# Kernel tuning notes

Hardware: AMD Instinct MI355X
Metric: run time of the kernel (lower is better)

Reference implementation:

```python
import jax, jax.numpy as jnp
import numpy as np

N, F, D = 32, 1024, 512
H = 2 * D  # dim * ratio
EPS = 1e-5


def batchnorm1d(x, gamma, beta):
    # x: (N, F, L); BatchNorm1d over channel dim F, stats over (N, L) (training mode, biased var)
    mean = jnp.mean(x, axis=(0, 2), keepdims=True)
    var = jnp.var(x, axis=(0, 2), keepdims=True)
    xn = (x - mean) * jax.lax.rsqrt(var + EPS)
    return xn * gamma[None, :, None] + beta[None, :, None]


def setup_inputs() -> dict:
    key = jax.random.key(0)
    ks = jax.random.split(key, 5)
    x = jax.random.normal(ks[0], (N, F, D), dtype=jnp.float32)
    W0 = jax.random.normal(ks[1], (H, D), dtype=jnp.float32) * 0.02  # Linear(D->H) weight (out,in)
    b0 = jnp.zeros((H,), jnp.float32)
    W1 = jax.random.normal(ks[2], (D, H), dtype=jnp.float32) * 0.02  # Linear(H->D)
    b1 = jnp.zeros((D,), jnp.float32)
    Wc = jax.random.normal(ks[3], (F, F), dtype=jnp.float32) * 0.02  # Conv1d k=1 weight (out_ch,in_ch)
    bc = jnp.zeros((F,), jnp.float32)
    ones = jnp.ones((F,), jnp.float32)
    zeros = jnp.zeros((F,), jnp.float32)
    return {
        "x": x,
        "W0": W0, "b0": b0, "g0": ones, "be0": zeros,
        "W1": W1, "b1": b1, "g1": ones, "be1": zeros,
        "gf": ones, "bf": zeros,
        "Wc": Wc, "bc": bc,
        "go": ones, "bo": zeros,
    }


def reference(x, W0, b0, g0, be0, W1, b1, g1, be1, gf, bf, Wc, bc, go, bo):
    # proj_mlp0: Linear(D->H) + BN1d(F)
    v = jnp.einsum('nfd,hd->nfh', x, W0) + b0  # (N, F, H)
    v = batchnorm1d(v, g0, be0)
    # correlation: bmm(v, v^T) -> softsign -> bmm(w, v)
    w = jnp.einsum('nfh,ngh->nfg', v, v)  # (N, F, F)
    w = w / (1.0 + jnp.abs(w))  # softsign
    v = jnp.einsum('nfg,ngh->nfh', w, v)  # (N, F, H)
    # proj_mlp1: Linear(H->D) + BN1d(F)
    v = jnp.einsum('nfh,dh->nfd', v, W1) + b1  # (N, F, D)
    v = batchnorm1d(v, g1, be1)
    # feed_norm(v + x)
    xr = batchnorm1d(v + x, gf, bf)
    # proj_conv: Conv1d(F->F, kernel=1) over channel dim
    v = jnp.einsum('oi,nid->nod', Wc, xr) + bc[None, :, None]
    return batchnorm1d(v + xr, go, bo)
```

## Files before the change

kernel.cpp:

```cpp
#include <hip/hip_runtime.h>
#include <stdint.h>

#define NB 32
#define FC 1024
#define DD 512
#define HH 1024
#define BN_EPS 1e-5f

typedef unsigned short u16;
typedef unsigned int u32;
typedef __attribute__((ext_vector_type(8))) short bf16x8;
typedef __attribute__((ext_vector_type(4))) float f32x4;
typedef __attribute__((ext_vector_type(8))) unsigned short ushort8v;

#define AS1 __attribute__((address_space(1)))
#define AS3 __attribute__((address_space(3)))

__device__ __forceinline__ float b2f(u16 u) {
    union { u32 i; float f; } v;
    v.i = ((u32)u) << 16;
    return v.f;
}
__device__ __forceinline__ u16 f2b(float f) {
    union { float f; u32 i; } v;
    v.f = f;
    const u32 b = v.i;
    return (u16)((b + 0x7FFFu + ((b >> 16) & 1u)) >> 16);
}

__device__ __forceinline__ void gld16(const u16* g, u16* l) {
    __builtin_amdgcn_global_load_lds((const AS1 u32*)g, (AS3 u32*)l, 16, 0, 0);
}

__device__ __forceinline__ void swizzle_tiles(int& mt, int& nt, int& zt) {
    const int gx = gridDim.x, gy = gridDim.y, gz = gridDim.z;
    const int mzTot = gy * gz;
    if ((mzTot & 7) != 0) { nt = blockIdx.x; mt = blockIdx.y; zt = blockIdx.z; return; }
    long lin = ((long)blockIdx.z * gy + blockIdx.y) * gx + blockIdx.x;
    const int slab = mzTot >> 3;
    const int xcd = (int)(lin & 7);
    const long idx = lin >> 3;
    nt = (int)(idx % gx);
    const int mz = (int)(idx / gx) + xcd * slab;
    mt = mz % gy;
    zt = mz / gy;
}

__global__ __launch_bounds__(256) void detect_dtype(
    const u32* __restrict__ x, int* __restrict__ flag)
{
    __shared__ int cnt[256];
    int c = 0;
    for (int i = threadIdx.x; i < 4096; i += 256) {
        const u32 lo = x[i] & 0xFFFFu;
        const u32 e = (lo >> 7) & 0xFFu;
        if (e >= 0x68u && e <= 0x85u) c++;
    }
    cnt[threadIdx.x] = c;
    __syncthreads();
    for (int s = 128; s > 0; s >>= 1) {
        if (threadIdx.x < (unsigned)s) cnt[threadIdx.x] += cnt[threadIdx.x + s];
        __syncthreads();
    }
    if (threadIdx.x == 0) flag[0] = (cnt[0] > 2048) ? 1 : 0;
}

__global__ __launch_bounds__(256) void zero_partials(float* __restrict__ sp) {
    sp[blockIdx.x * 256 + threadIdx.x] = 0.0f;
}

__global__ __launch_bounds__(256) void fold_bn(
    const float* __restrict__ sp, const u16* __restrict__ gamma,
    const u16* __restrict__ beta, float* __restrict__ ssf, float invCnt)
{
    const int f = blockIdx.x * 256 + threadIdx.x;
    if (f < FC) {
        const float mean = sp[f] * invCnt;
        const float var  = sp[FC + f] * invCnt - mean * mean;
        const float rstd = rsqrtf(var + BN_EPS);
        const float sc   = b2f(gamma[f]) * rstd;
        ssf[f]      = sc;
        ssf[FC + f] = b2f(beta[f]) - mean * sc;
    }
}

__global__ __launch_bounds__(256) void convert_to_bf16(
    const void* __restrict__ src, u16* __restrict__ dst, long n4,
    const int* __restrict__ flag)
{
    const bool isbf = (*flag != 0);
    long i4 = (long)blockIdx.x * blockDim.x + threadIdx.x;
    const long stride = (long)gridDim.x * blockDim.x;
    for (; i4 < n4; i4 += stride) {
        const long i = i4 << 2;
        if (isbf) {
            *(ushort4*)(dst + i) = *(const ushort4*)((const u16*)src + i);
        } else {
            const float4 v = *(const float4*)((const float*)src + i);
            ushort4 o;
            o.x = f2b(v.x); o.y = f2b(v.y); o.z = f2b(v.z); o.w = f2b(v.w);
            *(ushort4*)(dst + i) = o;
        }
    }
}

struct ConvArgs { const void* src[14]; long off[14]; long n4[14]; };
__global__ __launch_bounds__(256) void convert_params(
    ConvArgs a, u16* __restrict__ dst, const int* __restrict__ flag)
{
    const bool isbf = (*flag != 0);
    const long stride = (long)gridDim.x * blockDim.x;
    for (int s = 0; s < 14; ++s) {
        const long n4 = a.n4[s];
        u16* d = dst + a.off[s];
        const void* sp = a.src[s];
        for (long i4 = (long)blockIdx.x * blockDim.x + threadIdx.x; i4 < n4;
             i4 += stride) {
            const long i = i4 << 2;
            if (isbf) {
                *(ushort4*)(d + i) = *(const ushort4*)((const u16*)sp + i);
            } else {
                const float4 v = *(const float4*)((const float*)sp + i);
                ushort4 o;
                o.x = f2b(v.x); o.y = f2b(v.y); o.z = f2b(v.z); o.w = f2b(v.w);
                *(ushort4*)(d + i) = o;
            }
        }
    }
}

template<bool BIAS, bool SOFTSIGN, bool STATS, bool RESID>
__global__ __launch_bounds__(512, 4) void gemm128x256_nt(
    const u16* __restrict__ A, const u16* __restrict__ B,
    const u16* __restrict__ bias, const u16* __restrict__ resid,
    u16* __restrict__ C, float* __restrict__ sp,
    int M, int N, int K, int lda, int ldb, int ldc,
    long sA, long sB, long sC)
{
    extern __shared__ char smem[];

    int mt, nt, zt;
    swizzle_tiles(mt, nt, zt);
    const u16* Ab = A + (long)zt * sA + (long)(mt * 128) * lda;
    const u16* Bb = B + (long)zt * sB + (long)(nt * 256) * ldb;
    C += (long)zt * sC;
    const u16* RP = RESID ? (resid + (long)zt * sC) : nullptr;

    const int tid  = threadIdx.x;
    const int lane = tid & 63;
    const int wv   = tid >> 6;
    const int wrr  = (wv >> 2) * 64;
    const int wc   = (wv & 3) * 64;
    const int lm   = lane & 15;
    const int q    = lane >> 4;

    int aOff[4], bOff[4];
    #pragma unroll
    for (int i = 0; i < 4; ++i) {
        const int r = wrr + i * 16 + lm;
        aOff[i] = r * 64 + ((q ^ ((r >> 1) & 3)) << 4);
    }
    #pragma unroll
    for (int j = 0; j < 4; ++j) {
        const int r = wc + j * 16 + lm;
        bOff[j] = r * 64 + ((q ^ ((r >> 1) & 3)) << 4);
    }

    const int rw = lane >> 2, qs = lane & 3;
    const int rA  = wv * 16 + rw;
    const int rB0 = wv * 32 + rw;
    const int rB1 = wv * 32 + 16 + rw;
    const u16* pA  = Ab + (long)rA  * lda + ((qs ^ ((rA  >> 1) & 3)) << 3);
    const u16* pB0 = Bb + (long)rB0 * ldb + ((qs ^ ((rB0 >> 1) & 3)) << 3);
    const u16* pB1 = Bb + (long)rB1 * ldb + ((qs ^ ((rB1 >> 1) & 3)) << 3);
    const int ldsA  = wv * 1024;
    const int ldsB0 = wv * 2048;
    const int ldsB1 = wv * 2048 + 1024;

#define STAGE(bufOff, kofs) { \
    gld16(pA  + (kofs), (u16*)(smem + (bufOff) + ldsA)); \
    gld16(pB0 + (kofs), (u16*)(smem + (bufOff) + 8192 + ldsB0)); \
    gld16(pB1 + (kofs), (u16*)(smem + (bufOff) + 8192 + ldsB1)); }

    f32x4 acc[4][4] = {};

    const int NT = K >> 5;

    STAGE(0, 0);
    __syncthreads();

    for (int t = 0; t < NT; ++t) {
        const int bo = (t & 1) * 24576;
        const int bn = ((t + 1) & 1) * 24576;
        if (t + 1 < NT) STAGE(bn, (t + 1) * 32);

        bf16x8 a[4], b[4];
        const char* baseA = smem + bo;
        const char* baseB = smem + bo + 8192;
        #pragma unroll
        for (int i = 0; i < 4; ++i) a[i] = *(const bf16x8*)(baseA + aOff[i]);
        #pragma unroll
        for (int j = 0; j < 4; ++j) b[j] = *(const bf16x8*)(baseB + bOff[j]);

        #pragma unroll
        for (int i = 0; i < 4; ++i)
            #pragma unroll
            for (int j = 0; j < 4; ++j)
                acc[i][j] = __builtin_amdgcn_mfma_f32_16x16x32_bf16(
                    a[i], b[j], acc[i][j], 0, 0, 0);

        __syncthreads();
    }

#undef STAGE

    float* rep = (float*)smem + wv * (16 * 65);
    const int rr = lane >> 2;
    const int cg = lane & 3;
    const int m0 = mt * 128;
    const int n0 = nt * 256;
    #pragma unroll
    for (int i = 0; i < 4; ++i) {
        #pragma unroll
        for (int j = 0; j < 4; ++j) {
            const int col = 16 * j + lm;
            const float bj = BIAS ? b2f(bias[n0 + wc + col]) : 0.0f;
            #pragma unroll
            for (int r = 0; r < 4; ++r) {
                float v = acc[i][j][r] + bj;
                if (SOFTSIGN) v = v / (1.0f + fabsf(v));
                rep[(q * 4 + r) * 65 + col] = v;
            }
        }
        const int row = m0 + wrr + 16 * i + rr;
        const float* lr = rep + rr * 65 + cg * 16;
        float4 f0 = *(const float4*)(lr + 0);
        float4 f1 = *(const float4*)(lr + 4);
        float4 f2 = *(const float4*)(lr + 8);
        float4 f3 = *(const float4*)(lr + 12);
        if (RESID) {
            const u16* rp = RP + (long)row * ldc + n0 + wc + cg * 16;
            const ushort8v ra = *(const ushort8v*)rp;
            const ushort8v rb = *(const ushort8v*)(rp + 8);
            f0.x += b2f(ra[0]); f0.y += b2f(ra[1]); f0.z += b2f(ra[2]); f0.w += b2f(ra[3]);
            f1.x += b2f(ra[4]); f1.y += b2f(ra[5]); f1.z += b2f(ra[6]); f1.w += b2f(ra[7]);
            f2.x += b2f(rb[0]); f2.y += b2f(rb[1]); f2.z += b2f(rb[2]); f2.w += b2f(rb[3]);
            f3.x += b2f(rb[4]); f3.y += b2f(rb[5]); f3.z += b2f(rb[6]); f3.w += b2f(rb[7]);
        }
        if (STATS) {
            float s1 = (f0.x + f0.y + f0.z + f0.w) + (f1.x + f1.y + f1.z + f1.w)
                     + (f2.x + f2.y + f2.z + f2.w) + (f3.x + f3.y + f3.z + f3.w);
            float s2 = f0.x*f0.x + f0.y*f0.y + f0.z*f0.z + f0.w*f0.w
                     + f1.x*f1.x + f1.y*f1.y + f1.z*f1.z + f1.w*f1.w
                     + f2.x*f2.x + f2.y*f2.y + f2.z*f2.z + f2.w*f2.w
                     + f3.x*f3.x + f3.y*f3.y + f3.z*f3.z + f3.w*f3.w;
            s1 += __shfl_xor(s1, 1); s1 += __shfl_xor(s1, 2);
            s2 += __shfl_xor(s2, 1); s2 += __shfl_xor(s2, 2);
            if (cg == 0) {
                const int ch = row & (FC - 1);
                atomicAdd(&sp[ch], s1);
                atomicAdd(&sp[FC + ch], s2);
            }
        }
        ushort8v o0, o1;
        o0[0] = f2b(f0.x); o0[1] = f2b(f0.y); o0[2] = f2b(f0.z); o0[3] = f2b(f0.w);
        o0[4] = f2b(f1.x); o0[5] = f2b(f1.y); o0[6] = f2b(f1.z); o0[7] = f2b(f1.w);
        o1[0] = f2b(f2.x); o1[1] = f2b(f2.y); o1[2] = f2b(f2.z); o1[3] = f2b(f2.w);
        o1[4] = f2b(f3.x); o1[5] = f2b(f3.y); o1[6] = f2b(f3.z); o1[7] = f2b(f3.w);
        u16* cp = C + (long)row * ldc + n0 + wc + cg * 16;
        *(ushort8v*)cp = o0;
        *(ushort8v*)(cp + 8) = o1;
    }
}

__global__ __launch_bounds__(256) void transpose_bf16(
    const u16* __restrict__ src, u16* __restrict__ dst,
    int R, int Cc, long sS, long sD)
{
    __shared__ u16 t[32][33];
    const int bz = blockIdx.z;
    src += (long)bz * sS;
    dst += (long)bz * sD;
    const int c0 = blockIdx.x * 32;
    const int r0 = blockIdx.y * 32;
    const int lx = threadIdx.x & 31;
    const int ly = threadIdx.x >> 5;
    #pragma unroll
    for (int d = 0; d < 32; d += 8)
        t[ly + d][lx] = src[(long)(r0 + ly + d) * Cc + c0 + lx];
    __syncthreads();
    #pragma unroll
    for (int d = 0; d < 32; d += 8)
        dst[(long)(c0 + ly + d) * R + r0 + lx] = t[lx][ly + d];
}

__global__ __launch_bounds__(256) void transpose_bn_bf16(
    const u16* __restrict__ src, u16* __restrict__ dstT,
    u16* __restrict__ dstI, const float* __restrict__ ssf,
    int R, int Cc, long sS, long sD)
{
    __shared__ u16 t[32][33];
    const int bz = blockIdx.z;
    src  += (long)bz * sS;
    dstI += (long)bz * sS;
    dstT += (long)bz * sD;
    const int c0 = blockIdx.x * 32;
    const int r0 = blockIdx.y * 32;
    const int lx = threadIdx.x & 31;
    const int ly = threadIdx.x >> 5;
    #pragma unroll
    for (int d = 0; d < 32; d += 8) {
        const int r = r0 + ly + d;
        const u16 nv = f2b(fmaf(b2f(src[(long)r * Cc + c0 + lx]),
                                ssf[r], ssf[FC + r]));
        t[ly + d][lx] = nv;
        dstI[(long)r * Cc + c0 + lx] = nv;
    }
    __syncthreads();
    #pragma unroll
    for (int d = 0; d < 32; d += 8)
        dstT[(long)(c0 + ly + d) * R + r0 + lx] = t[lx][ly + d];
}

template<bool ADD, bool STATS>
__global__ __launch_bounds__(256) void bn_apply(
    const u16* __restrict__ src, const void* __restrict__ add,
    const int* __restrict__ addflag,
    const float* __restrict__ ss, void* __restrict__ dst,
    const int* __restrict__ outflag, long total4, int lcShift,
    float* __restrict__ sp)
{
    const bool addf32 = ADD && (addflag != nullptr) && (*addflag == 0);
    const bool outf32 = (outflag != nullptr) && (*outflag == 0);
    long i4 = (long)blockIdx.x * blockDim.x + threadIdx.x;
    const long stride = (long)gridDim.x * blockDim.x;
    for (; i4 < total4; i4 += stride) {
        const long i = i4 << 2;
        const int c = (int)((i >> lcShift) & (FC - 1));
        const float sc = ss[c];
        const float sh = ss[FC + c];
        const ushort4 v = *(const ushort4*)(src + i);
        float o0 = fmaf(b2f(v.x), sc, sh);
        float o1 = fmaf(b2f(v.y), sc, sh);
        float o2 = fmaf(b2f(v.z), sc, sh);
        float o3 = fmaf(b2f(v.w), sc, sh);
        if (ADD) {
            if (addf32) {
                const float4 a = *(const float4*)((const float*)add + i);
                o0 += a.x; o1 += a.y; o2 += a.z; o3 += a.w;
            } else {
                const ushort4 a = *(const ushort4*)((const u16*)add + i);
                o0 += b2f(a.x); o1 += b2f(a.y); o2 += b2f(a.z); o3 += b2f(a.w);
            }
        }
        if (STATS) {
            float s1 = o0 + o1 + o2 + o3;
            float s2 = o0 * o0 + o1 * o1 + o2 * o2 + o3 * o3;
            #pragma unroll
            for (int m = 1; m < 64; m <<= 1) {
                s1 += __shfl_xor(s1, m);
                s2 += __shfl_xor(s2, m);
            }
            if ((threadIdx.x & 63) == 0) {
                atomicAdd(&sp[c], s1);
                atomicAdd(&sp[FC + c], s2);
            }
        }
        if (outf32) {
            float4 o; o.x = o0; o.y = o1; o.z = o2; o.w = o3;
            *(float4*)((float*)dst + i) = o;
        } else {
            ushort4 o;
            o.x = f2b(o0); o.y = f2b(o1); o.z = f2b(o2); o.w = f2b(o3);
            *(ushort4*)((u16*)dst + i) = o;
        }
    }
}

extern "C" void kernel_launch(void* const* d_in, const int* in_sizes, int n_in,
                              void* d_out, int out_size, void* d_ws, size_t ws_size,
                              hipStream_t stream)
{
    const size_t MiB = (size_t)1 << 20;
    const long sFH = (long)FC * HH;
    const long sFF = (long)FC * FC;
    const long sFD = (long)FC * DD;
    const long PE  = (long)NB * FC * DD;

    const size_t GLDS = 49152;
    static bool s_attr = false;
    if (!s_attr) {
        s_attr = true;
        hipFuncSetAttribute(reinterpret_cast<const void*>(&gemm128x256_nt<true, false, true, false>),
                            hipFuncAttributeMaxDynamicSharedMemorySize, (int)GLDS);
        hipFuncSetAttribute(reinterpret_cast<const void*>(&gemm128x256_nt<false, true, false, false>),
                            hipFuncAttributeMaxDynamicSharedMemorySize, (int)GLDS);
        hipFuncSetAttribute(reinterpret_cast<const void*>(&gemm128x256_nt<false, false, false, false>),
                            hipFuncAttributeMaxDynamicSharedMemorySize, (int)GLDS);
        hipFuncSetAttribute(reinterpret_cast<const void*>(&gemm128x256_nt<true, false, true, true>),
                            hipFuncAttributeMaxDynamicSharedMemorySize, (int)GLDS);
    }

    long off[16];
    long cur = 0;
    for (int i = 1; i < 15; ++i) { off[i] = cur; cur += ((long)in_sizes[i] + 7) & ~7L; }
    const size_t paramBytes = (size_t)cur * 2;

    int cb = 32;
    while (cb > 1 &&
           64 * MiB + (size_t)cb * 6 * MiB + paramBytes + 65536 > ws_size)
        cb >>= 1;

    u16* V   = (u16*)d_ws;
    u16* VT  = (u16*)((char*)d_ws + 64 * MiB);
    u16* WW  = VT + (long)cb * sFH;
    u16* V2  = WW + (long)cb * sFF;
    u16* WC  = V2 + (long)cb * sFH;
    char* tail = (char*)(WC + cur);
    tail = (char*)(((uintptr_t)tail + 255) & ~(uintptr_t)255);
    float* SP0  = (float*)tail;
    float* SP1  = SP0 + 2 * FC;
    float* SP2  = SP1 + 2 * FC;
    float* SP3  = SP2 + 2 * FC;
    float* SSF  = SP3 + 2 * FC;
    int*   FLAG = (int*)(SSF + 2 * FC);
    u16* VX  = (u16*)d_out;
    u16* XB  = (u16*)d_out + PE;
    u16* V4  = V;
    u16* XRT = V + PE;

    const dim3 blk(256);
    const dim3 blk512(512);
    const dim3 egrid(4096);

    detect_dtype<<<1, blk, 0, stream>>>((const u32*)d_in[0], FLAG);
    zero_partials<<<dim3(32), blk, 0, stream>>>(SP0);
    ConvArgs ca;
    for (int i = 1; i < 15; ++i) {
        ca.src[i - 1] = d_in[i];
        ca.off[i - 1] = off[i];
        ca.n4[i - 1]  = (long)in_sizes[i] / 4;
    }
    convert_params<<<dim3(256), blk, 0, stream>>>(ca, WC, FLAG);
    convert_to_bf16<<<dim3(1024), blk, 0, stream>>>(d_in[0], XB, PE / 4, FLAG);

    const u16* W0c = WC + off[1];
    const u16* b0c = WC + off[2];
    const u16* g0c = WC + off[3];
    const u16* be0c = WC + off[4];
    const u16* W1c = WC + off[5];
    const u16* b1c = WC + off[6];
    const u16* g1c = WC + off[7];
    const u16* be1c = WC + off[8];
    const u16* gfc = WC + off[9];
    const u16* bfc = WC + off[10];
    const u16* Wcc = WC + off[11];
    const u16* bcc = WC + off[12];
    const u16* goc = WC + off[13];
    const u16* boc = WC + off[14];

    gemm128x256_nt<true, false, true, false><<<dim3(HH / 256, (NB * FC) / 128, 1), blk512, GLDS, stream>>>(
        XB, W0c, b0c, nullptr, V, SP0, NB * FC, HH, DD, DD, DD, HH, 0, 0, 0);
    fold_bn<<<dim3(4), blk, 0, stream>>>(SP0, g0c, be0c, SSF, 1.0f / (float)(NB * HH));

    for (int bz0 = 0; bz0 < NB; bz0 += cb) {
        const int c = (NB - bz0 < cb) ? (NB - bz0) : cb;
        transpose_bn_bf16<<<dim3(HH / 32, FC / 32, c), blk, 0, stream>>>(
            V + bz0 * sFH, VT, V + bz0 * sFH, SSF, FC, HH, sFH, sFH);
        gemm128x256_nt<false, true, false, false><<<dim3(FC / 256, FC / 128, c), blk512, GLDS, stream>>>(
            V + bz0 * sFH, V + bz0 * sFH, nullptr, nullptr, WW, nullptr,
            FC, FC, HH, HH, HH, FC, sFH, sFH, sFF);
        gemm128x256_nt<false, false, false, false><<<dim3(HH / 256, FC / 128, c), blk512, GLDS, stream>>>(
            WW, VT, nullptr, nullptr, V2, nullptr,
            FC, HH, FC, FC, FC, HH, sFF, sFH, sFH);
        gemm128x256_nt<true, false, true, false><<<dim3(DD / 256, (c * FC) / 128, 1), blk512, GLDS, stream>>>(
            V2, W1c, b1c, nullptr, VX + bz0 * sFD, SP1,
            c * FC, DD, HH, HH, HH, DD, 0, 0, 0);
    }
    fold_bn<<<dim3(4), blk, 0, stream>>>(SP1, g1c, be1c, SSF, 1.0f / (float)(NB * DD));

    bn_apply<true, true><<<egrid, blk, 0, stream>>>(
        VX, XB, nullptr, SSF, VX, nullptr, PE / 4, 9, SP2);
    fold_bn<<<dim3(4), blk, 0, stream>>>(SP2, gfc, bfc, SSF, 1.0f / (float)(NB * DD));

    bn_apply<false, false><<<egrid, blk, 0, stream>>>(
        VX, nullptr, nullptr, SSF, VX, nullptr, PE / 4, 9, nullptr);

    transpose_bf16<<<dim3(DD / 32, FC / 32, NB), blk, 0, stream>>>(
        VX, XRT, FC, DD, sFD, sFD);
    gemm128x256_nt<true, false, true, true><<<dim3(DD / 256, FC / 128, NB), blk512, GLDS, stream>>>(
        Wcc, XRT, bcc, VX, V4, SP3, FC, DD, FC, FC, FC, DD, 0, sFD, sFD);
    fold_bn<<<dim3(4), blk, 0, stream>>>(SP3, goc, boc, SSF, 1.0f / (float)(NB * DD));

    bn_apply<false, false><<<egrid, blk, 0, stream>>>(
        V4, nullptr, nullptr, SSF, d_out, FLAG, PE / 4, 9, nullptr);
}
```

Measured before the change: 609.9 us.

## Exploit Gram symmetry, triple-buffer GEMM pipeline, fuse BN apply into transpose

The v·v^T correlation GEMM now computes only lower-triangular tiles and a small mirror kernel copies them into the upper blocks, skipping roughly 40% of that GEMM's tiles. The GEMM main loop goes from double to triple-buffered LDS with a partial vmcnt wait, so loads run two stages ahead, at the cost of 72KB of LDS per block, which may reduce occupancy. The standalone BN-apply pass before the final conv is folded into transpose_bn_bf16, removing one elementwise pass over the activations. The mirror kernel adds a launch and extra writes per chunk.

```diff
diff --git a/kernel.cpp b/kernel.cpp
--- a/kernel.cpp
+++ b/kernel.cpp
@@ -133,7 +133,7 @@
 __global__ __launch_bounds__(512, 4) void gemm128x256_nt(
     const u16* __restrict__ A, const u16* __restrict__ B,
     const u16* __restrict__ bias, const u16* __restrict__ resid,
-    u16* __restrict__ C, float* __restrict__ sp,
+    u16* __restrict__ C, float* __restrict__ sp, int sym,
     int M, int N, int K, int lda, int ldb, int ldc,
     long sA, long sB, long sC)
 {
@@ -141,6 +141,7 @@
 
     int mt, nt, zt;
     swizzle_tiles(mt, nt, zt);
+    if (sym && mt < 2 * nt) return;
     const u16* Ab = A + (long)zt * sA + (long)(mt * 128) * lda;
     const u16* Bb = B + (long)zt * sB + (long)(nt * 256) * ldb;
     C += (long)zt * sC;
@@ -182,17 +183,26 @@
     gld16(pB0 + (kofs), (u16*)(smem + (bufOff) + 8192 + ldsB0)); \
     gld16(pB1 + (kofs), (u16*)(smem + (bufOff) + 8192 + ldsB1)); }
 
+#define RINGBAR() { \
+    asm volatile("s_waitcnt vmcnt(3) lgkmcnt(0)" ::: "memory"); \
+    __builtin_amdgcn_sched_barrier(0); \
+    __builtin_amdgcn_s_barrier(); \
+    __builtin_amdgcn_sched_barrier(0); }
+
     f32x4 acc[4][4] = {};
 
     const int NT = K >> 5;
 
     STAGE(0, 0);
-    __syncthreads();
-
+    STAGE(24576, 32);
+    RINGBAR();
+
+    int cur = 0, nxt = 2;
     for (int t = 0; t < NT; ++t) {
-        const int bo = (t & 1) * 24576;
-        const int bn = ((t + 1) & 1) * 24576;
-        if (t + 1 < NT) STAGE(bn, (t + 1) * 32);
+        const int bo = cur * 24576;
+        const int bn = nxt * 24576;
+        const int kn = (((t + 2) < NT) ? (t + 2) : (NT - 1)) * 32;
+        STAGE(bn, kn);
 
         bf16x8 a[4], b[4];
         const char* baseA = smem + bo;
@@ -209,10 +219,17 @@
                 acc[i][j] = __builtin_amdgcn_mfma_f32_16x16x32_bf16(
                     a[i], b[j], acc[i][j], 0, 0, 0);
 
-        __syncthreads();
+        RINGBAR();
+        cur = (cur == 2) ? 0 : cur + 1;
+        nxt = (nxt == 2) ? 0 : nxt + 1;
     }
 
 #undef STAGE
+#undef RINGBAR
+
+    asm volatile("s_waitcnt vmcnt(0)" ::: "memory");
+    __builtin_amdgcn_sched_barrier(0);
+    __syncthreads();
 
     float* rep = (float*)smem + wv * (16 * 65);
     const int rr = lane >> 2;
@@ -273,25 +290,27 @@
     }
 }
 
-__global__ __launch_bounds__(256) void transpose_bf16(
-    const u16* __restrict__ src, u16* __restrict__ dst,
-    int R, int Cc, long sS, long sD)
-{
+__global__ __launch_bounds__(256) void mirror_upper(
+    u16* __restrict__ W, long sW)
+{
+    const int MTt[12] = {0,1, 0,1,2,3, 0,1,2,3,4,5};
+    const int NTt[12] = {1,1, 2,2,2,2, 3,3,3,3,3,3};
     __shared__ u16 t[32][33];
-    const int bz = blockIdx.z;
-    src += (long)bz * sS;
-    dst += (long)bz * sD;
-    const int c0 = blockIdx.x * 32;
-    const int r0 = blockIdx.y * 32;
+    const int id = blockIdx.y;
+    const int mt = MTt[id], nt = NTt[id];
+    W += (long)blockIdx.z * sW;
+    const int rb = blockIdx.x & 3, cb = blockIdx.x >> 2;
+    const int dr0 = mt * 128 + rb * 32;
+    const int dc0 = nt * 256 + cb * 32;
     const int lx = threadIdx.x & 31;
     const int ly = threadIdx.x >> 5;
     #pragma unroll
     for (int d = 0; d < 32; d += 8)
-        t[ly + d][lx] = src[(long)(r0 + ly + d) * Cc + c0 + lx];
+        t[ly + d][lx] = W[(long)(dc0 + ly + d) * FC + dr0 + lx];
     __syncthreads();
     #pragma unroll
     for (int d = 0; d < 32; d += 8)
-        dst[(long)(c0 + ly + d) * R + r0 + lx] = t[lx][ly + d];
+        W[(long)(dr0 + ly + d) * FC + dc0 + lx] = t[lx][ly + d];
 }
 
 __global__ __launch_bounds__(256) void transpose_bn_bf16(
@@ -387,7 +406,7 @@
     const long sFD = (long)FC * DD;
     const long PE  = (long)NB * FC * DD;
 
-    const size_t GLDS = 49152;
+    const size_t GLDS = 73728;
     static bool s_attr = false;
     if (!s_attr) {
         s_attr = true;
@@ -460,7 +479,7 @@
     const u16* boc = WC + off[14];
 
     gemm128x256_nt<true, false, true, false><<<dim3(HH / 256, (NB * FC) / 128, 1), blk512, GLDS, stream>>>(
-        XB, W0c, b0c, nullptr, V, SP0, NB * FC, HH, DD, DD, DD, HH, 0, 0, 0);
+        XB, W0c, b0c, nullptr, V, SP0, 0, NB * FC, HH, DD, DD, DD, HH, 0, 0, 0);
     fold_bn<<<dim3(4), blk, 0, stream>>>(SP0, g0c, be0c, SSF, 1.0f / (float)(NB * HH));
 
     for (int bz0 = 0; bz0 < NB; bz0 += cb) {
@@ -468,13 +487,14 @@
         transpose_bn_bf16<<<dim3(HH / 32, FC / 32, c), blk, 0, stream>>>(
             V + bz0 * sFH, VT, V + bz0 * sFH, SSF, FC, HH, sFH, sFH);
         gemm128x256_nt<false, true, false, false><<<dim3(FC / 256, FC / 128, c), blk512, GLDS, stream>>>(
-            V + bz0 * sFH, V + bz0 * sFH, nullptr, nullptr, WW, nullptr,
+            V + bz0 * sFH, V + bz0 * sFH, nullptr, nullptr, WW, nullptr, 1,
             FC, FC, HH, HH, HH, FC, sFH, sFH, sFF);
+        mirror_upper<<<dim3(32, 12, c), blk, 0, stream>>>(WW, sFF);
         gemm128x256_nt<false, false, false, false><<<dim3(HH / 256, FC / 128, c), blk512, GLDS, stream>>>(
-            WW, VT, nullptr, nullptr, V2, nullptr,
+            WW, VT, nullptr, nullptr, V2, nullptr, 0,
             FC, HH, FC, FC, FC, HH, sFF, sFH, sFH);
         gemm128x256_nt<true, false, true, false><<<dim3(DD / 256, (c * FC) / 128, 1), blk512, GLDS, stream>>>(
-            V2, W1c, b1c, nullptr, VX + bz0 * sFD, SP1,
+            V2, W1c, b1c, nullptr, VX + bz0 * sFD, SP1, 0,
             c * FC, DD, HH, HH, HH, DD, 0, 0, 0);
     }
     fold_bn<<<dim3(4), blk, 0, stream>>>(SP1, g1c, be1c, SSF, 1.0f / (float)(NB * DD));
@@ -483,13 +503,11 @@
         VX, XB, nullptr, SSF, VX, nullptr, PE / 4, 9, SP2);
     fold_bn<<<dim3(4), blk, 0, stream>>>(SP2, gfc, bfc, SSF, 1.0f / (float)(NB * DD));
 
-    bn_apply<false, false><<<egrid, blk, 0, stream>>>(
-        VX, nullptr, nullptr, SSF, VX, nullptr, PE / 4, 9, nullptr);
-
-    transpose_bf16<<<dim3(DD / 32, FC / 32, NB), blk, 0, stream>>>(
-        VX, XRT, FC, DD, sFD, sFD);
+    transpose_bn_bf16<<<dim3(DD / 32, FC / 32, NB), blk, 0, stream>>>(
+        VX, XRT, VX, SSF, FC, DD, sFD, sFD);
+
     gemm128x256_nt<true, false, true, true><<<dim3(DD / 256, FC / 128, NB), blk512, GLDS, stream>>>(
-        Wcc, XRT, bcc, VX, V4, SP3, FC, DD, FC, FC, FC, DD, 0, sFD, sFD);
+        Wcc, XRT, bcc, VX, V4, SP3, 0, FC, DD, FC, FC, FC, DD, 0, sFD, sFD);
     fold_bn<<<dim3(4), blk, 0, stream>>>(SP3, goc, boc, SSF, 1.0f / (float)(NB * DD));
 
     bn_apply<false, false><<<egrid, blk, 0, stream>>>(
```

Measured after the change: 617.4 us. No clear change (+1.2%).
